# Performance work log

Measured on AMD Instinct MI355X. Metric: run time of the kernel, lower is better.

Reference implementation:

```python
import jax, jax.numpy as jnp
import numpy as np
import math

DIM = 1024
NUM_HEADS = 8
HEAD_DIM = DIM // NUM_HEADS
B, T, K_T, K_A, K_P = 8, 1024, 512, 64, 64
LN_EPS = 1e-5


def setup_inputs() -> dict:
    key = jax.random.key(0)
    ks = jax.random.split(key, 16)
    s = 1.0 / math.sqrt(DIM)
    inp = {
        "x": jax.random.normal(ks[0], (B, T, DIM), jnp.float32),
        "h_t": jax.random.normal(ks[1], (B, K_T, DIM), jnp.float32),
        "h_a": jax.random.normal(ks[2], (B, K_A, DIM), jnp.float32),
        "p": jax.random.normal(ks[3], (B, K_P, DIM), jnp.float32),
        "Wq": jax.random.normal(ks[4], (DIM, DIM), jnp.float32) * s,
        "bq": jnp.zeros((DIM,), jnp.float32),
        "Wk": jax.random.normal(ks[5], (DIM, DIM), jnp.float32) * s,
        "bk": jnp.zeros((DIM,), jnp.float32),
        "Wv": jax.random.normal(ks[6], (DIM, DIM), jnp.float32) * s,
        "bv": jnp.zeros((DIM,), jnp.float32),
        "Wo": jax.random.normal(ks[7], (DIM, DIM), jnp.float32) * s,
        "bo": jnp.zeros((DIM,), jnp.float32),
        "gating_factor": jnp.zeros((1,), jnp.float32) + 0.1,
        "ln_g": jnp.ones((DIM,), jnp.float32),
        "ln_b": jnp.zeros((DIM,), jnp.float32),
        "Wf": jax.random.normal(ks[8], (DIM, DIM), jnp.float32) * s,
        "bf": jnp.zeros((DIM,), jnp.float32),
    }
    return inp


def _heads(t):  # [B,S,C] -> [B,H,S,D]
    Bx, S, _ = t.shape
    return t.reshape(Bx, S, NUM_HEADS, HEAD_DIM).transpose(0, 2, 1, 3)


def reference(x, h_t, h_a, p, Wq, bq, Wk, bk, Wv, bv, Wo, bo,
              gating_factor, ln_g, ln_b, Wf, bf):
    ratio_g = jnp.tanh(gating_factor)  # shape (1,)
    h = jnp.concatenate([h_a, p], axis=1)  # [B, K_a, C]

    q = _heads(x @ Wq.T + bq)                 # [B,H,T,D]
    k_tok = _heads(x @ Wk.T + bk)
    v_tok = _heads(x @ Wv.T + bv)
    k_act = _heads(h @ Wk.T + bk)
    v_act = _heads(h @ Wv.T + bv)
    k_tsk = _heads(h_t @ Wk.T + bk)
    v_tsk = _heads(h_t @ Wv.T + bv)

    s_tok = jnp.einsum('bhtd,bhsd->bhts', q, k_tok)
    s_act = jnp.einsum('bhtd,bhsd->bhts', q, k_act)
    s_tsk = jnp.einsum('bhtd,bhsd->bhts', q, k_tsk) * ratio_g
    scores = jnp.concatenate([s_tok, s_act, s_tsk], axis=-1) / math.sqrt(HEAD_DIM)
    attn = jax.nn.softmax(scores, axis=-1)  # [B,H,T,T+Ka+Kt]

    v_all = jnp.concatenate([v_tok, v_act, v_tsk], axis=2)  # [B,H,S_all,D]
    out = jnp.einsum('bhts,bhsd->bhtd', attn, v_all)
    out = out.transpose(0, 2, 1, 3).reshape(x.shape)  # [B,T,C]
    out = out @ Wo.T + bo

    y = out + x
    mu = jnp.mean(y, axis=-1, keepdims=True)
    var = jnp.mean(jnp.square(y - mu), axis=-1, keepdims=True)
    y = (y - mu) * jax.lax.rsqrt(var + LN_EPS) * ln_g + ln_b
    y = y @ Wf.T + bf
    return jax.nn.relu(y)
```

## Files before the change

### kernel.cpp

```cpp
#include <hip/hip_runtime.h>
#include <hip/hip_bf16.h>
#include <math.h>

typedef unsigned short u16;
typedef __attribute__((ext_vector_type(8))) short s16x8;
typedef __attribute__((ext_vector_type(4))) float f32x4;
typedef __attribute__((ext_vector_type(16))) float f32x16;
typedef __attribute__((ext_vector_type(4))) unsigned short u16x4;

__device__ __forceinline__ u16 f2bf(float f) {
  union { float f; unsigned u; } v; v.f = f;
  unsigned r = (v.u + 0x7FFFu + ((v.u >> 16) & 1u)) >> 16;
  return (u16)r;
}

__device__ __forceinline__ void gload16(const void* g, void* l) {
  __builtin_amdgcn_global_load_lds((const __attribute__((address_space(1))) unsigned int*)g,
                                   (__attribute__((address_space(3))) unsigned int*)l, 16, 0, 0);
}

__device__ __forceinline__ unsigned cvt_pk_bf16(float a, float b) {
  unsigned r;
  asm("v_cvt_pk_bf16_f32 %0, %1, %2" : "=v"(r) : "v"(a), "v"(b));
  return r;
}


__global__ __launch_bounds__(256) void cvt_weights(
    const float* __restrict__ wq, const float* __restrict__ wk, const float* __restrict__ wv,
    const float* __restrict__ wo, const float* __restrict__ wf,
    u16* __restrict__ wqkv, u16* __restrict__ wobf, u16* __restrict__ wfbf)
{
  int i = blockIdx.x * 256 + threadIdx.x;
  int which = i >> 18;
  int idx = i & 262143;
  const float* src = which==0 ? wq : which==1 ? wk : which==2 ? wv : which==3 ? wo : wf;
  float4 v = ((const float4*)src)[idx];
  u16x4 o = { f2bf(v.x), f2bf(v.y), f2bf(v.z), f2bf(v.w) };
  u16* dst = which < 3 ? (wqkv + (size_t)which*1048576) : (which==3 ? wobf : wfbf);
  ((u16x4*)dst)[idx] = o;
}

__global__ __launch_bounds__(256) void build_m(
    const float* __restrict__ x, const float* __restrict__ ht,
    const float* __restrict__ ha, const float* __restrict__ p,
    u16* __restrict__ M)
{
  int row = blockIdx.x; int t = threadIdx.x;
  int b = row / 1664, s = row % 1664;
  const float* src;
  if (s < 1024)      src = x  + (size_t)(b*1024 + s)*1024;
  else if (s < 1088) src = ha + (size_t)(b*64 + (s-1024))*1024;
  else if (s < 1152) src = p  + (size_t)(b*64 + (s-1088))*1024;
  else               src = ht + (size_t)(b*512 + (s-1152))*1024;
  float4 v = ((const float4*)src)[t];
  u16x4 o = { f2bf(v.x), f2bf(v.y), f2bf(v.z), f2bf(v.w) };
  ((u16x4*)(M + (size_t)row*1024))[t] = o;
}


template<int EPI>
__global__ __launch_bounds__(256) void gemm_bt(
    const u16* __restrict__ A, const u16* __restrict__ Bw, int K,
    const float* __restrict__ bias0, const float* __restrict__ bias1, const float* __restrict__ bias2,
    const void* p0, void* p1, void* p2, void* p3)
{
  __shared__ __align__(16) u16 As[128*32];
  __shared__ __align__(16) u16 Bs[128*32];
  const int tid = threadIdx.x;
  const int l = tid & 63;
  const int w = tid >> 6;
  const int m0 = blockIdx.x * 128;
  const int n0 = blockIdx.y * 128;

  if constexpr (EPI == 0) {
    if (n0 < 1024 && (m0 % 1664) >= 1024) return;
  }

  const int wr = w >> 1, wc = w & 1;
  const int l15 = l & 15, lg = l >> 4;

  f32x4 acc[4][4];
  #pragma unroll
  for (int i=0;i<4;++i)
    #pragma unroll
    for (int j=0;j<4;++j) acc[i][j] = (f32x4){0,0,0,0};

  const int kiters = K >> 5;
  for (int kt = 0; kt < kiters; ++kt) {
    __syncthreads();
    #pragma unroll
    for (int c = 0; c < 2; ++c) {
      const int rbase = w*32 + c*16;
      const int rl = rbase + (l >> 2);
      const int kb = kt*32 + (l & 3)*8;
      gload16(A  + (size_t)(m0 + rl)*K + kb, (void*)(As + rbase*32));
      gload16(Bw + (size_t)(n0 + rl)*K + kb, (void*)(Bs + rbase*32));
    }
    __syncthreads();
    s16x8 av[4];
    #pragma unroll
    for (int mi=0;mi<4;++mi)
      av[mi] = *(const s16x8*)(As + (wr*64 + mi*16 + l15)*32 + lg*8);
    #pragma unroll
    for (int ni=0;ni<4;++ni) {
      s16x8 bv = *(const s16x8*)(Bs + (wc*64 + ni*16 + l15)*32 + lg*8);
      #pragma unroll
      for (int mi=0;mi<4;++mi)
        acc[mi][ni] = __builtin_amdgcn_mfma_f32_16x16x32_bf16(av[mi], bv, acc[mi][ni], 0,0,0);
    }
  }

  float ratio = 0.f;
  if constexpr (EPI == 0) ratio = tanhf(((const float*)p0)[0]);

  #pragma unroll
  for (int mi=0;mi<4;++mi) {
    #pragma unroll
    for (int ni=0;ni<4;++ni) {
      #pragma unroll
      for (int r=0;r<4;++r) {
        const int row = m0 + wr*64 + mi*16 + lg*4 + r;
        const int col = n0 + wc*64 + ni*16 + l15;
        if constexpr (EPI == 0) {
          const int b = row / 1664, s = row % 1664;
          if (col < 1024) {
            float v = acc[mi][ni][r] + bias0[col];
            if (s < 1024)
              ((u16*)p1)[(size_t)(b*1024 + s)*1024 + col] = f2bf(v * 0.08838834764831845f);
          } else if (col < 2048) {
            float v = acc[mi][ni][r] + bias1[col-1024];
            if (s >= 1152) v *= ratio;
            ((u16*)p2)[(size_t)row*1024 + (col-1024)] = f2bf(v);
          } else {
            float v = acc[mi][ni][r] + bias2[col-2048];
            ((u16*)p3)[(size_t)row*1024 + (col-2048)] = f2bf(v);
          }
        } else if constexpr (EPI == 1) {
          float v = acc[mi][ni][r] + bias0[col] + ((const float*)p0)[(size_t)row*1024 + col];
          ((float*)p1)[(size_t)row*1024 + col] = v;
        } else {
          float v = acc[mi][ni][r] + bias0[col];
          ((float*)p1)[(size_t)row*1024 + col] = fmaxf(v, 0.f);
        }
      }
    }
  }
}


__global__ __launch_bounds__(256) void vtrans(
    const u16* __restrict__ V, u16* __restrict__ Vt)
{
  __shared__ u16 Ls[64][68];
  const int st = blockIdx.x, dt = blockIdx.y, b = blockIdx.z;
  const int t = threadIdx.x;
  const int rq = t >> 4, c4 = t & 15;
  #pragma unroll
  for (int i=0;i<4;++i) {
    const int r = i*16 + rq;
    u16x4 v = *(const u16x4*)(V + ((size_t)(b*1664 + st*64 + r))*1024 + dt*64 + c4*4);
    Ls[r][c4*4+0] = v[0]; Ls[r][c4*4+1] = v[1]; Ls[r][c4*4+2] = v[2]; Ls[r][c4*4+3] = v[3];
  }
  __syncthreads();
  #pragma unroll
  for (int i=0;i<4;++i) {
    const int dr = i*16 + rq;
    u16x4 ov = { Ls[c4*4+0][dr], Ls[c4*4+1][dr], Ls[c4*4+2][dr], Ls[c4*4+3][dr] };
    *(u16x4*)(Vt + ((size_t)(b*1024 + dt*64 + dr))*1664 + st*64 + c4*4) = ov;
  }
}


__global__ __launch_bounds__(256, 2) void flash_attn(
    const u16* __restrict__ Q, const u16* __restrict__ Kb, const u16* __restrict__ Vtg,
    u16* __restrict__ O)
{
  __shared__ __align__(16) u16 Kl[2][64*128];
  __shared__ __align__(16) u16 Vl[2][128*64];

  const int tid = threadIdx.x;
  const int l = tid & 63;
  const int w = tid >> 6;
  const int l31 = l & 31;
  const int hi = l >> 5;
  const int bh = blockIdx.x & 63;
  const int qt = blockIdx.x >> 6;
  const int b = bh >> 3, h = bh & 7;
  const int colh = h * 128;
  const int q0 = qt*128 + w*32;

  s16x8 qf[8];
  {
    const size_t qrow = (size_t)(b*1024 + q0 + l31)*1024 + colh;
    #pragma unroll
    for (int kc=0;kc<8;++kc)
      qf[kc] = *(const s16x8*)(Q + qrow + kc*16 + hi*8);
  }

  f32x16 oacc[4];
  #pragma unroll
  for (int dt2=0;dt2<4;++dt2)
    #pragma unroll
    for (int i=0;i<16;++i) oacc[dt2][i] = 0.f;
  float m_run = -INFINITY, l_run = 0.f;

  const size_t kbase  = (size_t)(b*1664)*1024 + colh;
  const size_t vtbase = (size_t)(b*1024 + colh)*1664;

  auto stage = [&](int st, int nb) {
    const int s0 = st*64;
    #pragma unroll
    for (int i=0;i<4;++i) {
      const int e = i*256 + tid;
      const int sl = e >> 4, c = e & 15;
      const int g = (c & 8) | ((c ^ sl) & 7);
      gload16(Kb + kbase + (size_t)(s0 + sl)*1024 + g*8,
              (void*)(Kl[nb] + (i*256 + w*64)*8));
    }
    #pragma unroll
    for (int i=0;i<4;++i) {
      const int e = i*256 + tid;
      const int d = e >> 3, c3 = e & 7;
      const int g3 = (c3 ^ d) & 7;
      gload16(Vtg + vtbase + (size_t)d*1664 + s0 + g3*8,
              (void*)(Vl[nb] + (i*256 + w*64)*8));
    }
  };

  stage(0, 0);
  __syncthreads();
  int cur = 0;

  for (int st=0; st<26; ++st) {
    if (st + 1 < 26) stage(st + 1, cur ^ 1);

    f32x16 sacc[2];
    #pragma unroll
    for (int stile=0; stile<2; ++stile) {
      #pragma unroll
      for (int i=0;i<16;++i) sacc[stile][i] = 0.f;
      #pragma unroll
      for (int kc=0; kc<8; ++kc) {
        const int sl = stile*32 + l31;
        const int gc = kc*2 + hi;
        const int cl = (gc & 8) | ((gc ^ sl) & 7);
        s16x8 kf = *(const s16x8*)(Kl[cur] + sl*128 + cl*8);
        sacc[stile] = __builtin_amdgcn_mfma_f32_32x32x16_bf16(kf, qf[kc], sacc[stile], 0,0,0);
      }
    }

    float tm[8];
    #pragma unroll
    for (int i=0;i<8;++i)
      tm[i] = fmaxf(fmaxf(sacc[0][i], sacc[0][i+8]), fmaxf(sacc[1][i], sacc[1][i+8]));
    float pm = fmaxf(fmaxf(fmaxf(tm[0],tm[1]), fmaxf(tm[2],tm[3])),
                     fmaxf(fmaxf(tm[4],tm[5]), fmaxf(tm[6],tm[7])));
    pm = fmaxf(pm, __shfl_xor(pm, 32));

    if (__any(pm > m_run + 8.f)) {
      const float mnew = fmaxf(m_run, pm);
      const float alpha = __expf(m_run - mnew);
      m_run = mnew;
      l_run *= alpha;
      #pragma unroll
      for (int r=0;r<16;++r) {
        const int qr = (r&3) + 8*(r>>2) + 4*hi;
        const float ar = __shfl(alpha, qr);
        #pragma unroll
        for (int dt2=0;dt2<4;++dt2) oacc[dt2][r] *= ar;
      }
    }

    float ps = 0.f;
    #pragma unroll
    for (int stile=0; stile<2; ++stile)
      #pragma unroll
      for (int i=0;i<16;++i) {
        const float v = __expf(sacc[stile][i] - m_run);
        sacc[stile][i] = v;
        ps += v;
      }
    ps += __shfl_xor(ps, 32);
    l_run += ps;

    s16x8 pf[4];
    #pragma unroll
    for (int kc2=0; kc2<4; ++kc2) {
      const int stile = kc2 >> 1;
      const int rb = (kc2 & 1) * 8;
      const unsigned A = cvt_pk_bf16(sacc[stile][rb+0], sacc[stile][rb+1]);
      const unsigned B = cvt_pk_bf16(sacc[stile][rb+2], sacc[stile][rb+3]);
      const unsigned C = cvt_pk_bf16(sacc[stile][rb+4], sacc[stile][rb+5]);
      const unsigned D = cvt_pk_bf16(sacc[stile][rb+6], sacc[stile][rb+7]);
      const unsigned x1 = (unsigned)__shfl_xor((int)(hi ? A : C), 32);
      const unsigned x2 = (unsigned)__shfl_xor((int)(hi ? B : D), 32);
      union { unsigned u[4]; s16x8 v; } fr;
      fr.u[0] = hi ? x1 : A;
      fr.u[1] = hi ? x2 : B;
      fr.u[2] = hi ? C : x1;
      fr.u[3] = hi ? D : x2;
      pf[kc2] = fr.v;
    }

    #pragma unroll
    for (int dt2=0; dt2<4; ++dt2) {
      const int d = dt2*32 + l31;
      #pragma unroll
      for (int kc2=0; kc2<4; ++kc2) {
        const int g3 = kc2*2 + hi;
        const int cl3 = (g3 ^ d) & 7;
        s16x8 vf = *(const s16x8*)(Vl[cur] + d*64 + cl3*8);
        oacc[dt2] = __builtin_amdgcn_mfma_f32_32x32x16_bf16(pf[kc2], vf, oacc[dt2], 0,0,0);
      }
    }

    __syncthreads();
    cur ^= 1;
  }

  const float linv = 1.f / l_run;
  #pragma unroll
  for (int r=0;r<16;++r) {
    const int qr = (r&3) + 8*(r>>2) + 4*hi;
    const float lr = __shfl(linv, qr);
    const size_t row = (size_t)(b*1024 + q0 + qr)*1024 + colh;
    #pragma unroll
    for (int dt2=0;dt2<4;++dt2)
      O[row + dt2*32 + l31] = f2bf(oacc[dt2][r] * lr);
  }
}


__global__ __launch_bounds__(256) void ln_kernel(
    const float* __restrict__ y, const float* __restrict__ g, const float* __restrict__ bb,
    u16* __restrict__ out)
{
  const int row = blockIdx.x, t = threadIdx.x;
  float4 v = ((const float4*)y)[row*256 + t];
  float s  = v.x + v.y + v.z + v.w;
  float s2 = v.x*v.x + v.y*v.y + v.z*v.z + v.w*v.w;
  #pragma unroll
  for (int off=1; off<64; off<<=1) { s += __shfl_xor(s, off); s2 += __shfl_xor(s2, off); }
  __shared__ float ps[4], ps2[4];
  const int w = t >> 6;
  if ((t & 63) == 0) { ps[w] = s; ps2[w] = s2; }
  __syncthreads();
  s  = ps[0] + ps[1] + ps[2] + ps[3];
  s2 = ps2[0] + ps2[1] + ps2[2] + ps2[3];
  const float mu = s * (1.f/1024.f);
  const float var = s2 * (1.f/1024.f) - mu*mu;
  const float rs = rsqrtf(var + 1e-5f);
  float4 gg = ((const float4*)g)[t];
  float4 bv = ((const float4*)bb)[t];
  u16x4 o = { f2bf((v.x-mu)*rs*gg.x + bv.x),
              f2bf((v.y-mu)*rs*gg.y + bv.y),
              f2bf((v.z-mu)*rs*gg.z + bv.z),
              f2bf((v.w-mu)*rs*gg.w + bv.w) };
  ((u16x4*)out)[row*256 + t] = o;
}


extern "C" void kernel_launch(void* const* d_in, const int* in_sizes, int n_in,
                              void* d_out, int out_size, void* d_ws, size_t ws_size,
                              hipStream_t stream)
{
  (void)in_sizes; (void)n_in; (void)out_size; (void)ws_size;
  const float* x   = (const float*)d_in[0];
  const float* ht  = (const float*)d_in[1];
  const float* ha  = (const float*)d_in[2];
  const float* pp  = (const float*)d_in[3];
  const float* Wq  = (const float*)d_in[4];
  const float* bq  = (const float*)d_in[5];
  const float* Wk  = (const float*)d_in[6];
  const float* bk  = (const float*)d_in[7];
  const float* Wv  = (const float*)d_in[8];
  const float* bv  = (const float*)d_in[9];
  const float* Wo  = (const float*)d_in[10];
  const float* bo  = (const float*)d_in[11];
  const float* gat = (const float*)d_in[12];
  const float* lng = (const float*)d_in[13];
  const float* lnb = (const float*)d_in[14];
  const float* Wf  = (const float*)d_in[15];
  const float* bfp = (const float*)d_in[16];
  float* out = (float*)d_out;

  char* ws = (char*)d_ws;
  size_t off = 0;
  auto alloc = [&](size_t bytes) { void* r = ws + off; off += (bytes + 255) & ~255ull; return r; };
  u16* M    = (u16*)alloc(13312ull*1024*2);
  u16* Wqkv = (u16*)alloc(3072ull*1024*2);
  u16* Wobf = (u16*)alloc(1024ull*1024*2);
  u16* Wfbf = (u16*)alloc(1024ull*1024*2);
  u16* Qb   = (u16*)alloc(8192ull*1024*2);
  u16* Kb2  = (u16*)alloc(13312ull*1024*2);
  u16* Vb2  = (u16*)alloc(13312ull*1024*2);
  u16* Ab   = (u16*)alloc(8192ull*1024*2);
  u16* Vtg  = M;
  float* Y  = (float*)M;
  u16* Ln   = Qb;

  hipLaunchKernelGGL(cvt_weights, dim3(5120), dim3(256), 0, stream,
                     Wq, Wk, Wv, Wo, Wf, Wqkv, Wobf, Wfbf);
  hipLaunchKernelGGL(build_m, dim3(13312), dim3(256), 0, stream, x, ht, ha, pp, M);
  hipLaunchKernelGGL((gemm_bt<0>), dim3(104, 24), dim3(256), 0, stream,
                     M, Wqkv, 1024, bq, bk, bv,
                     (const void*)gat, (void*)Qb, (void*)Kb2, (void*)Vb2);
  hipLaunchKernelGGL(vtrans, dim3(26, 16, 8), dim3(256), 0, stream, Vb2, Vtg);
  hipLaunchKernelGGL(flash_attn, dim3(512), dim3(256), 0, stream, Qb, Kb2, Vtg, Ab);
  hipLaunchKernelGGL((gemm_bt<1>), dim3(64, 8), dim3(256), 0, stream,
                     Ab, Wobf, 1024, bo, nullptr, nullptr,
                     (const void*)x, (void*)Y, nullptr, nullptr);
  hipLaunchKernelGGL(ln_kernel, dim3(8192), dim3(256), 0, stream, Y, lng, lnb, Ln);
  hipLaunchKernelGGL((gemm_bt<2>), dim3(64, 8), dim3(256), 0, stream,
                     Ln, Wfbf, 1024, bfp, nullptr, nullptr,
                     nullptr, (void*)out, nullptr, nullptr);
}
```

Measured before the change: 489.6 us.

## Replace QKV projection with 256x256 double-buffered pipelined MFMA GEMM kernel

Adds a dedicated QKV projection kernel that uses 256x256 tiles with 512 threads, a two-stage LDS ring buffer with XOR-swizzled layout, and interleaved prefetch/compute phases with explicit waitcnt/barrier and setprio. It also remaps blocks with a swizzle and skips Q tiles that fall entirely in the non-token rows. The aim is to raise MFMA utilisation and data reuse over the previous 128x128 single-buffered GEMM and to hide global load latency. The cost is heavy hand-tuned synchronisation that is fragile and sensitive to register pressure and occupancy, with some wasted work on tiles that only partly overlap the token rows.

```diff
diff --git a/kernel.cpp b/kernel.cpp
--- a/kernel.cpp
+++ b/kernel.cpp
@@ -59,11 +59,142 @@
 }
 
 
+#define PHASE(D, QM, QN, STAGE_STMT, ENDSYNC)                                    \
+  {                                                                              \
+    s16x8 af_[4][2], bf_[2][2];                                                  \
+    _Pragma("unroll")                                                            \
+    for (int mi2=0; mi2<4; ++mi2) {                                              \
+      const int r = wm*128 + (QM*4+mi2)*16 + l15;                                \
+      _Pragma("unroll")                                                          \
+      for (int ks=0; ks<2; ++ks)                                                 \
+        af_[mi2][ks] = *(const s16x8*)(As[D] + r*64 + (((ks*4+lg) ^ (r&7))<<3)); \
+    }                                                                            \
+    _Pragma("unroll")                                                            \
+    for (int ni2=0; ni2<2; ++ni2) {                                              \
+      const int r = wn*64 + (QN*2+ni2)*16 + l15;                                 \
+      _Pragma("unroll")                                                          \
+      for (int ks=0; ks<2; ++ks)                                                 \
+        bf_[ni2][ks] = *(const s16x8*)(Bs[D] + r*64 + (((ks*4+lg) ^ (r&7))<<3)); \
+    }                                                                            \
+    STAGE_STMT;                                                                  \
+    __builtin_amdgcn_s_barrier();                                                \
+    asm volatile("s_waitcnt lgkmcnt(0)" ::: "memory");                           \
+    __builtin_amdgcn_s_setprio(1);                                               \
+    _Pragma("unroll")                                                            \
+    for (int mi2=0; mi2<4; ++mi2)                                                \
+      _Pragma("unroll")                                                          \
+      for (int ni2=0; ni2<2; ++ni2)                                              \
+        _Pragma("unroll")                                                        \
+        for (int ks=0; ks<2; ++ks)                                               \
+          acc[QM*4+mi2][QN*2+ni2] = __builtin_amdgcn_mfma_f32_16x16x32_bf16(     \
+              af_[mi2][ks], bf_[ni2][ks], acc[QM*4+mi2][QN*2+ni2], 0,0,0);       \
+    __builtin_amdgcn_s_setprio(0);                                               \
+    ENDSYNC;                                                                     \
+  }
+
+__global__ __launch_bounds__(512, 2) void gemm256_qkv(
+    const u16* __restrict__ A, const u16* __restrict__ Bw,
+    const float* __restrict__ bias_q, const float* __restrict__ bias_k,
+    const float* __restrict__ bias_v, const float* __restrict__ gat,
+    u16* __restrict__ Qb, u16* __restrict__ Kb, u16* __restrict__ Vb)
+{
+  __shared__ __align__(16) u16 As[2][256*64];
+  __shared__ __align__(16) u16 Bs[2][256*64];
+
+  const int tid = threadIdx.x;
+  const int l = tid & 63;
+  const int w = tid >> 6;
+  const int wm = w >> 2, wn = w & 3;
+  const int l15 = l & 15, lg = l >> 4;
+  const int w8 = w * 8;
+
+  const int b0 = blockIdx.x;
+  const int swz = (b0 & 7) * 78 + (b0 >> 3);
+  const int mt = swz % 52, nt = swz / 52;
+  const int m0 = mt * 256, n0 = nt * 256;
+
+  if (n0 < 1024) {
+    const int s0 = m0 % 1664;
+    if (s0 >= 1024 && s0 <= 1408) return;
+  }
+
+  auto stA = [&](int d, int h, int kt) {
+    #pragma unroll
+    for (int i=0;i<2;++i) {
+      const int r0 = i*128 + h*64 + w8;
+      const int r  = r0 + (l >> 3);
+      const int sck = (l & 7) ^ (r & 7);
+      gload16(A + (size_t)(m0 + r)*1024 + kt*64 + sck*8, (void*)(As[d] + r0*64));
+    }
+  };
+  auto stB = [&](int d, int h, int kt) {
+    #pragma unroll
+    for (int i=0;i<2;++i) {
+      const int blk = i*2 + (w>>2);
+      const int r0 = (w&3)*8 + blk*64 + h*32;
+      const int r  = r0 + (l >> 3);
+      const int sck = (l & 7) ^ (r & 7);
+      gload16(Bw + (size_t)(n0 + r)*1024 + kt*64 + sck*8, (void*)(Bs[d] + r0*64));
+    }
+  };
+
+  f32x4 acc[8][4];
+  #pragma unroll
+  for (int i=0;i<8;++i)
+    #pragma unroll
+    for (int j=0;j<4;++j) acc[i][j] = (f32x4){0,0,0,0};
+
+  stB(0,0,0); stA(0,1,0); stA(0,0,0); stB(0,1,0); stB(1,0,1); stA(1,1,1);
+  asm volatile("s_waitcnt vmcnt(4)\ns_barrier" ::: "memory");
+
+  for (int t = 0; t < 16; ++t) {
+    const int d = t & 1;
+    const int e = d ^ 1;
+    PHASE(d, 0, 0, if (t+1 < 16) stA(e, 0, t+1), __builtin_amdgcn_s_barrier())
+    PHASE(d, 1, 0, if (t+1 < 16) stB(e, 1, t+1),
+          asm volatile("s_waitcnt vmcnt(8)\ns_barrier" ::: "memory"))
+    PHASE(d, 1, 1, if (t+2 < 16) stB(d, 0, t+2), __builtin_amdgcn_s_barrier())
+    PHASE(d, 0, 1, if (t+2 < 16) stA(d, 1, t+2), )
+    if (t <= 13)      asm volatile("s_waitcnt vmcnt(6)\ns_barrier" ::: "memory");
+    else if (t == 14) asm volatile("s_waitcnt vmcnt(0)\ns_barrier" ::: "memory");
+    else              __builtin_amdgcn_s_barrier();
+  }
+
+  const float ratio = tanhf(gat[0]);
+  #pragma unroll
+  for (int mi=0;mi<8;++mi) {
+    #pragma unroll
+    for (int ni=0;ni<4;++ni) {
+      #pragma unroll
+      for (int rr=0;rr<4;++rr) {
+        const int row = m0 + wm*128 + mi*16 + lg*4 + rr;
+        const int col = n0 + wn*64 + ni*16 + l15;
+        const int b = row / 1664, s = row % 1664;
+        const float a = acc[mi][ni][rr];
+        if (col < 1024) {
+          if (s < 1024) {
+            float v = a + bias_q[col];
+            Qb[(size_t)(b*1024 + s)*1024 + col] = f2bf(v * 0.08838834764831845f);
+          }
+        } else if (col < 2048) {
+          float v = a + bias_k[col-1024];
+          if (s >= 1152) v *= ratio;
+          Kb[(size_t)row*1024 + (col-1024)] = f2bf(v);
+        } else {
+          float v = a + bias_v[col-2048];
+          Vb[(size_t)row*1024 + (col-2048)] = f2bf(v);
+        }
+      }
+    }
+  }
+}
+
+
 template<int EPI>
 __global__ __launch_bounds__(256) void gemm_bt(
     const u16* __restrict__ A, const u16* __restrict__ Bw, int K,
-    const float* __restrict__ bias0, const float* __restrict__ bias1, const float* __restrict__ bias2,
-    const void* p0, void* p1, void* p2, void* p3)
+    const float* __restrict__ bias0,
+    const void* p0, void* p1)
 {
   __shared__ __align__(16) u16 As[128*32];
   __shared__ __align__(16) u16 Bs[128*32];
@@ -73,10 +204,6 @@
   const int m0 = blockIdx.x * 128;
   const int n0 = blockIdx.y * 128;
 
-  if constexpr (EPI == 0) {
-    if (n0 < 1024 && (m0 % 1664) >= 1024) return;
-  }
-
   const int wr = w >> 1, wc = w & 1;
   const int l15 = l & 15, lg = l >> 4;
 
@@ -111,9 +238,6 @@
     }
   }
 
-  float ratio = 0.f;
-  if constexpr (EPI == 0) ratio = tanhf(((const float*)p0)[0]);
-
   #pragma unroll
   for (int mi=0;mi<4;++mi) {
     #pragma unroll
@@ -122,21 +246,7 @@
       for (int r=0;r<4;++r) {
         const int row = m0 + wr*64 + mi*16 + lg*4 + r;
         const int col = n0 + wc*64 + ni*16 + l15;
-        if constexpr (EPI == 0) {
-          const int b = row / 1664, s = row % 1664;
-          if (col < 1024) {
-            float v = acc[mi][ni][r] + bias0[col];
-            if (s < 1024)
-              ((u16*)p1)[(size_t)(b*1024 + s)*1024 + col] = f2bf(v * 0.08838834764831845f);
-          } else if (col < 2048) {
-            float v = acc[mi][ni][r] + bias1[col-1024];
-            if (s >= 1152) v *= ratio;
-            ((u16*)p2)[(size_t)row*1024 + (col-1024)] = f2bf(v);
-          } else {
-            float v = acc[mi][ni][r] + bias2[col-2048];
-            ((u16*)p3)[(size_t)row*1024 + (col-2048)] = f2bf(v);
-          }
-        } else if constexpr (EPI == 1) {
+        if constexpr (EPI == 1) {
           float v = acc[mi][ni][r] + bias0[col] + ((const float*)p0)[(size_t)row*1024 + col];
           ((float*)p1)[(size_t)row*1024 + col] = v;
         } else {
@@ -403,16 +513,13 @@
   hipLaunchKernelGGL(cvt_weights, dim3(5120), dim3(256), 0, stream,
                      Wq, Wk, Wv, Wo, Wf, Wqkv, Wobf, Wfbf);
   hipLaunchKernelGGL(build_m, dim3(13312), dim3(256), 0, stream, x, ht, ha, pp, M);
-  hipLaunchKernelGGL((gemm_bt<0>), dim3(104, 24), dim3(256), 0, stream,
-                     M, Wqkv, 1024, bq, bk, bv,
-                     (const void*)gat, (void*)Qb, (void*)Kb2, (void*)Vb2);
+  hipLaunchKernelGGL(gemm256_qkv, dim3(624), dim3(512), 0, stream,
+                     M, Wqkv, bq, bk, bv, gat, Qb, Kb2, Vb2);
   hipLaunchKernelGGL(vtrans, dim3(26, 16, 8), dim3(256), 0, stream, Vb2, Vtg);
   hipLaunchKernelGGL(flash_attn, dim3(512), dim3(256), 0, stream, Qb, Kb2, Vtg, Ab);
   hipLaunchKernelGGL((gemm_bt<1>), dim3(64, 8), dim3(256), 0, stream,
-                     Ab, Wobf, 1024, bo, nullptr, nullptr,
-                     (const void*)x, (void*)Y, nullptr, nullptr);
+                     Ab, Wobf, 1024, bo, (const void*)x, (void*)Y);
   hipLaunchKernelGGL(ln_kernel, dim3(8192), dim3(256), 0, stream, Y, lng, lnb, Ln);
   hipLaunchKernelGGL((gemm_bt<2>), dim3(64, 8), dim3(256), 0, stream,
-                     Ln, Wfbf, 1024, bfp, nullptr, nullptr,
-                     nullptr, (void*)out, nullptr, nullptr);
-}
+                     Ln, Wfbf, 1024, bfp, nullptr, (void*)out);
+}
```

Measured after the change: 487.0 us. About the same (-0.5%).

## Add triple-buffered swizzled QKV GEMM with XCD-aware tile mapping

Applied to the files above, without the earlier changes.

Replaces the generic QKV projection GEMM with a dedicated kernel. It uses triple-buffered LDS staging with asynchronous global-to-LDS loads issued two k-steps ahead, an XOR-swizzled LDS layout to avoid bank conflicts, s_setprio around the MFMA block, and a block-to-tile remap that groups M tiles per XCD for L2 reuse. The goal is to hide load latency and remove the two full barriers per k-iteration in the old loop. In exchange it uses more LDS per block, which can limit occupancy.

```diff
diff --git a/kernel.cpp b/kernel.cpp
--- a/kernel.cpp
+++ b/kernel.cpp
@@ -59,11 +59,124 @@
 }
 
 
+__global__ __launch_bounds__(256, 3) void gemm128_qkv(
+    const u16* __restrict__ A, const u16* __restrict__ Bw,
+    const float* __restrict__ bias_q, const float* __restrict__ bias_k,
+    const float* __restrict__ bias_v, const float* __restrict__ gat,
+    u16* __restrict__ Qb, u16* __restrict__ Kb, u16* __restrict__ Vb)
+{
+  __shared__ __align__(16) u16 As3[3][128*32];
+  __shared__ __align__(16) u16 Bs3[3][128*32];
+
+  const int tid = threadIdx.x;
+  const int l = tid & 63;
+  const int w = tid >> 6;
+  const int wr = w >> 1, wc = w & 1;
+  const int l15 = l & 15, lg = l >> 4;
+
+  const int b0 = blockIdx.x;
+  const int xcd = b0 & 7;
+  const int loc = b0 >> 3;
+  const int g = loc / 52, r5 = loc % 52;
+  const int mt = xcd*13 + (r5 % 13);
+  const int nt = g*4 + (r5 / 13);
+  const int m0 = mt * 128, n0 = nt * 128;
+
+  if (n0 < 1024 && (m0 % 1664) >= 1024) return;
+
+  auto stage = [&](int kt, int sb) {
+    #pragma unroll
+    for (int i=0;i<2;++i) {
+      const int e = i*256 + tid;
+      const int rr = e >> 2, c2 = e & 3;
+      const int gch = c2 ^ ((rr >> 1) & 3);
+      gload16(A + (size_t)(m0 + rr)*1024 + kt*32 + gch*8,
+              (void*)(As3[sb] + (i*256 + w*64)*8));
+    }
+    #pragma unroll
+    for (int i=0;i<2;++i) {
+      const int e = i*256 + tid;
+      const int rr = e >> 2, c2 = e & 3;
+      const int gch = c2 ^ ((rr >> 1) & 3);
+      gload16(Bw + (size_t)(n0 + rr)*1024 + kt*32 + gch*8,
+              (void*)(Bs3[sb] + (i*256 + w*64)*8));
+    }
+  };
+
+  f32x4 acc[4][4];
+  #pragma unroll
+  for (int i=0;i<4;++i)
+    #pragma unroll
+    for (int j=0;j<4;++j) acc[i][j] = (f32x4){0,0,0,0};
+
+  stage(0, 0); stage(1, 1);
+  asm volatile("s_waitcnt vmcnt(4)\ns_barrier" ::: "memory");
+
+  int cur = 0;
+  for (int t = 0; t < 32; ++t) {
+    const int sb = cur >= 1 ? cur - 1 : 2;
+    if (t + 2 < 32) stage(t + 2, sb);
+
+    s16x8 af[4], bf[4];
+    #pragma unroll
+    for (int mi=0;mi<4;++mi) {
+      const int rr = wr*64 + mi*16 + l15;
+      af[mi] = *(const s16x8*)(As3[cur] + rr*32 + ((lg ^ ((rr>>1)&3))<<3));
+    }
+    #pragma unroll
+    for (int ni=0;ni<4;++ni) {
+      const int rr = wc*64 + ni*16 + l15;
+      bf[ni] = *(const s16x8*)(Bs3[cur] + rr*32 + ((lg ^ ((rr>>1)&3))<<3));
+    }
+
+    __builtin_amdgcn_s_setprio(1);
+    #pragma unroll
+    for (int mi=0;mi<4;++mi)
+      #pragma unroll
+      for (int ni=0;ni<4;++ni)
+        acc[mi][ni] = __builtin_amdgcn_mfma_f32_16x16x32_bf16(af[mi], bf[ni], acc[mi][ni], 0,0,0);
+    __builtin_amdgcn_s_setprio(0);
+
+    if (t < 30)       asm volatile("s_waitcnt vmcnt(4)\ns_barrier" ::: "memory");
+    else if (t == 30) asm volatile("s_waitcnt vmcnt(0)\ns_barrier" ::: "memory");
+    cur = cur == 2 ? 0 : cur + 1;
+  }
+
+  const float ratio = tanhf(gat[0]);
+  #pragma unroll
+  for (int mi=0;mi<4;++mi) {
+    #pragma unroll
+    for (int ni=0;ni<4;++ni) {
+      #pragma unroll
+      for (int rr=0;rr<4;++rr) {
+        const int row = m0 + wr*64 + mi*16 + lg*4 + rr;
+        const int col = n0 + wc*64 + ni*16 + l15;
+        const int b = row / 1664, s = row % 1664;
+        const float a = acc[mi][ni][rr];
+        if (col < 1024) {
+          if (s < 1024) {
+            float v = a + bias_q[col];
+            Qb[(size_t)(b*1024 + s)*1024 + col] = f2bf(v * 0.08838834764831845f);
+          }
+        } else if (col < 2048) {
+          float v = a + bias_k[col-1024];
+          if (s >= 1152) v *= ratio;
+          Kb[(size_t)row*1024 + (col-1024)] = f2bf(v);
+        } else {
+          float v = a + bias_v[col-2048];
+          Vb[(size_t)row*1024 + (col-2048)] = f2bf(v);
+        }
+      }
+    }
+  }
+}
+
+
 template<int EPI>
 __global__ __launch_bounds__(256) void gemm_bt(
     const u16* __restrict__ A, const u16* __restrict__ Bw, int K,
-    const float* __restrict__ bias0, const float* __restrict__ bias1, const float* __restrict__ bias2,
-    const void* p0, void* p1, void* p2, void* p3)
+    const float* __restrict__ bias0,
+    const void* p0, void* p1)
 {
   __shared__ __align__(16) u16 As[128*32];
   __shared__ __align__(16) u16 Bs[128*32];
@@ -73,10 +186,6 @@
   const int m0 = blockIdx.x * 128;
   const int n0 = blockIdx.y * 128;
 
-  if constexpr (EPI == 0) {
-    if (n0 < 1024 && (m0 % 1664) >= 1024) return;
-  }
-
   const int wr = w >> 1, wc = w & 1;
   const int l15 = l & 15, lg = l >> 4;
 
@@ -111,9 +220,6 @@
     }
   }
 
-  float ratio = 0.f;
-  if constexpr (EPI == 0) ratio = tanhf(((const float*)p0)[0]);
-
   #pragma unroll
   for (int mi=0;mi<4;++mi) {
     #pragma unroll
@@ -122,21 +228,7 @@
       for (int r=0;r<4;++r) {
         const int row = m0 + wr*64 + mi*16 + lg*4 + r;
         const int col = n0 + wc*64 + ni*16 + l15;
-        if constexpr (EPI == 0) {
-          const int b = row / 1664, s = row % 1664;
-          if (col < 1024) {
-            float v = acc[mi][ni][r] + bias0[col];
-            if (s < 1024)
-              ((u16*)p1)[(size_t)(b*1024 + s)*1024 + col] = f2bf(v * 0.08838834764831845f);
-          } else if (col < 2048) {
-            float v = acc[mi][ni][r] + bias1[col-1024];
-            if (s >= 1152) v *= ratio;
-            ((u16*)p2)[(size_t)row*1024 + (col-1024)] = f2bf(v);
-          } else {
-            float v = acc[mi][ni][r] + bias2[col-2048];
-            ((u16*)p3)[(size_t)row*1024 + (col-2048)] = f2bf(v);
-          }
-        } else if constexpr (EPI == 1) {
+        if constexpr (EPI == 1) {
           float v = acc[mi][ni][r] + bias0[col] + ((const float*)p0)[(size_t)row*1024 + col];
           ((float*)p1)[(size_t)row*1024 + col] = v;
         } else {
@@ -403,16 +495,13 @@
   hipLaunchKernelGGL(cvt_weights, dim3(5120), dim3(256), 0, stream,
                      Wq, Wk, Wv, Wo, Wf, Wqkv, Wobf, Wfbf);
   hipLaunchKernelGGL(build_m, dim3(13312), dim3(256), 0, stream, x, ht, ha, pp, M);
-  hipLaunchKernelGGL((gemm_bt<0>), dim3(104, 24), dim3(256), 0, stream,
-                     M, Wqkv, 1024, bq, bk, bv,
-                     (const void*)gat, (void*)Qb, (void*)Kb2, (void*)Vb2);
+  hipLaunchKernelGGL(gemm128_qkv, dim3(2496), dim3(256), 0, stream,
+                     M, Wqkv, bq, bk, bv, gat, Qb, Kb2, Vb2);
   hipLaunchKernelGGL(vtrans, dim3(26, 16, 8), dim3(256), 0, stream, Vb2, Vtg);
   hipLaunchKernelGGL(flash_attn, dim3(512), dim3(256), 0, stream, Qb, Kb2, Vtg, Ab);
   hipLaunchKernelGGL((gemm_bt<1>), dim3(64, 8), dim3(256), 0, stream,
-                     Ab, Wobf, 1024, bo, nullptr, nullptr,
-                     (const void*)x, (void*)Y, nullptr, nullptr);
+                     Ab, Wobf, 1024, bo, (const void*)x, (void*)Y);
   hipLaunchKernelGGL(ln_kernel, dim3(8192), dim3(256), 0, stream, Y, lng, lnb, Ln);
   hipLaunchKernelGGL((gemm_bt<2>), dim3(64, 8), dim3(256), 0, stream,
-                     Ln, Wfbf, 1024, bfp, nullptr, nullptr,
-                     nullptr, (void*)out, nullptr, nullptr);
-}
+                     Ln, Wfbf, 1024, bfp, nullptr, (void*)out);
+}
```

New measurement: 425.9 us. 13.0% less time.

## Double-buffer GEMM LDS tiles with swizzle and XCD-aware block mapping

Applied to the files above, without the earlier changes.

Rewrites the bf16 GEMM kernel so the next K-slice is loaded into a second LDS buffer while MFMAs run on the current one, which halves the barriers per iteration. It also XOR-swizzles the LDS layout to reduce bank conflicts, raises MFMA wave priority, and remaps the flat block index so each XCD works on a contiguous group of M tiles, improving L2 reuse. LDS use doubles, which may lower occupancy, and K is now hard-coded to 1024.

```diff
diff --git a/kernel.cpp b/kernel.cpp
--- a/kernel.cpp
+++ b/kernel.cpp
@@ -60,25 +60,53 @@
 
 
 template<int EPI>
-__global__ __launch_bounds__(256) void gemm_bt(
-    const u16* __restrict__ A, const u16* __restrict__ Bw, int K,
-    const float* __restrict__ bias0, const float* __restrict__ bias1, const float* __restrict__ bias2,
-    const void* p0, void* p1, void* p2, void* p3)
-{
-  __shared__ __align__(16) u16 As[128*32];
-  __shared__ __align__(16) u16 Bs[128*32];
+__global__ __launch_bounds__(256, 5) void gemm128(
+    const u16* __restrict__ A, const u16* __restrict__ Bw,
+    const float* __restrict__ bias0, const float* __restrict__ bias1,
+    const float* __restrict__ bias2, const float* __restrict__ gat,
+    void* o0, void* o1, void* o2, const float* __restrict__ resid,
+    int mpx, int ng)
+{
+  __shared__ __align__(16) u16 As2[2][128*32];
+  __shared__ __align__(16) u16 Bs2[2][128*32];
+
   const int tid = threadIdx.x;
   const int l = tid & 63;
   const int w = tid >> 6;
-  const int m0 = blockIdx.x * 128;
-  const int n0 = blockIdx.y * 128;
+  const int wr = w >> 1, wc = w & 1;
+  const int l15 = l & 15, lg = l >> 4;
+
+  const int b0 = blockIdx.x;
+  const int xcd = b0 & 7;
+  const int loc = b0 >> 3;
+  const int chunk = mpx * ng;
+  const int g = loc / chunk, r5 = loc % chunk;
+  const int mt = xcd*mpx + (r5 % mpx);
+  const int nt = g*ng + (r5 / mpx);
+  const int m0 = mt * 128, n0 = nt * 128;
 
   if constexpr (EPI == 0) {
     if (n0 < 1024 && (m0 % 1664) >= 1024) return;
   }
 
-  const int wr = w >> 1, wc = w & 1;
-  const int l15 = l & 15, lg = l >> 4;
+  auto stage = [&](int kt, int sb) {
+    #pragma unroll
+    for (int i=0;i<2;++i) {
+      const int e = i*256 + tid;
+      const int rr = e >> 2, c2 = e & 3;
+      const int gch = c2 ^ ((rr >> 1) & 3);
+      gload16(A + (size_t)(m0 + rr)*1024 + kt*32 + gch*8,
+              (void*)(As2[sb] + (i*256 + w*64)*8));
+    }
+    #pragma unroll
+    for (int i=0;i<2;++i) {
+      const int e = i*256 + tid;
+      const int rr = e >> 2, c2 = e & 3;
+      const int gch = c2 ^ ((rr >> 1) & 3);
+      gload16(Bw + (size_t)(n0 + rr)*1024 + kt*32 + gch*8,
+              (void*)(Bs2[sb] + (i*256 + w*64)*8));
+    }
+  };
 
   f32x4 acc[4][4];
   #pragma unroll
@@ -86,62 +114,69 @@
     #pragma unroll
     for (int j=0;j<4;++j) acc[i][j] = (f32x4){0,0,0,0};
 
-  const int kiters = K >> 5;
-  for (int kt = 0; kt < kiters; ++kt) {
-    __syncthreads();
-    #pragma unroll
-    for (int c = 0; c < 2; ++c) {
-      const int rbase = w*32 + c*16;
-      const int rl = rbase + (l >> 2);
-      const int kb = kt*32 + (l & 3)*8;
-      gload16(A  + (size_t)(m0 + rl)*K + kb, (void*)(As + rbase*32));
-      gload16(Bw + (size_t)(n0 + rl)*K + kb, (void*)(Bs + rbase*32));
-    }
-    __syncthreads();
-    s16x8 av[4];
+  stage(0, 0);
+  asm volatile("s_waitcnt vmcnt(0)\ns_barrier" ::: "memory");
+
+  for (int t = 0; t < 32; ++t) {
+    const int cur = t & 1;
+    if (t + 1 < 32) stage(t + 1, cur ^ 1);
+
+    s16x8 af[4], bf[4];
+    #pragma unroll
+    for (int mi=0;mi<4;++mi) {
+      const int rr = wr*64 + mi*16 + l15;
+      af[mi] = *(const s16x8*)(As2[cur] + rr*32 + ((lg ^ ((rr>>1)&3))<<3));
+    }
+    #pragma unroll
+    for (int ni=0;ni<4;++ni) {
+      const int rr = wc*64 + ni*16 + l15;
+      bf[ni] = *(const s16x8*)(Bs2[cur] + rr*32 + ((lg ^ ((rr>>1)&3))<<3));
+    }
+
+    __builtin_amdgcn_s_setprio(1);
     #pragma unroll
     for (int mi=0;mi<4;++mi)
-      av[mi] = *(const s16x8*)(As + (wr*64 + mi*16 + l15)*32 + lg*8);
+      #pragma unroll
+      for (int ni=0;ni<4;++ni)
+        acc[mi][ni] = __builtin_amdgcn_mfma_f32_16x16x32_bf16(af[mi], bf[ni], acc[mi][ni], 0,0,0);
+    __builtin_amdgcn_s_setprio(0);
+
+    if (t < 31) asm volatile("s_waitcnt vmcnt(0)\ns_barrier" ::: "memory");
+  }
+
+  float ratio = 0.f;
+  if constexpr (EPI == 0) ratio = tanhf(gat[0]);
+
+  #pragma unroll
+  for (int mi=0;mi<4;++mi) {
     #pragma unroll
     for (int ni=0;ni<4;++ni) {
-      s16x8 bv = *(const s16x8*)(Bs + (wc*64 + ni*16 + l15)*32 + lg*8);
-      #pragma unroll
-      for (int mi=0;mi<4;++mi)
-        acc[mi][ni] = __builtin_amdgcn_mfma_f32_16x16x32_bf16(av[mi], bv, acc[mi][ni], 0,0,0);
-    }
-  }
-
-  float ratio = 0.f;
-  if constexpr (EPI == 0) ratio = tanhf(((const float*)p0)[0]);
-
-  #pragma unroll
-  for (int mi=0;mi<4;++mi) {
-    #pragma unroll
-    for (int ni=0;ni<4;++ni) {
-      #pragma unroll
-      for (int r=0;r<4;++r) {
-        const int row = m0 + wr*64 + mi*16 + lg*4 + r;
+      #pragma unroll
+      for (int rr=0;rr<4;++rr) {
+        const int row = m0 + wr*64 + mi*16 + lg*4 + rr;
         const int col = n0 + wc*64 + ni*16 + l15;
+        const float a = acc[mi][ni][rr];
         if constexpr (EPI == 0) {
           const int b = row / 1664, s = row % 1664;
           if (col < 1024) {
-            float v = acc[mi][ni][r] + bias0[col];
-            if (s < 1024)
-              ((u16*)p1)[(size_t)(b*1024 + s)*1024 + col] = f2bf(v * 0.08838834764831845f);
+            if (s < 1024) {
+              float v = a + bias0[col];
+              ((u16*)o0)[(size_t)(b*1024 + s)*1024 + col] = f2bf(v * 0.08838834764831845f);
+            }
           } else if (col < 2048) {
-            float v = acc[mi][ni][r] + bias1[col-1024];
+            float v = a + bias1[col-1024];
             if (s >= 1152) v *= ratio;
-            ((u16*)p2)[(size_t)row*1024 + (col-1024)] = f2bf(v);
+            ((u16*)o1)[(size_t)row*1024 + (col-1024)] = f2bf(v);
           } else {
-            float v = acc[mi][ni][r] + bias2[col-2048];
-            ((u16*)p3)[(size_t)row*1024 + (col-2048)] = f2bf(v);
+            float v = a + bias2[col-2048];
+            ((u16*)o2)[(size_t)row*1024 + (col-2048)] = f2bf(v);
           }
         } else if constexpr (EPI == 1) {
-          float v = acc[mi][ni][r] + bias0[col] + ((const float*)p0)[(size_t)row*1024 + col];
-          ((float*)p1)[(size_t)row*1024 + col] = v;
+          float v = a + bias0[col] + resid[(size_t)row*1024 + col];
+          ((float*)o0)[(size_t)row*1024 + col] = v;
         } else {
-          float v = acc[mi][ni][r] + bias0[col];
-          ((float*)p1)[(size_t)row*1024 + col] = fmaxf(v, 0.f);
+          float v = a + bias0[col];
+          ((float*)o0)[(size_t)row*1024 + col] = fmaxf(v, 0.f);
         }
       }
     }
@@ -403,16 +438,16 @@
   hipLaunchKernelGGL(cvt_weights, dim3(5120), dim3(256), 0, stream,
                      Wq, Wk, Wv, Wo, Wf, Wqkv, Wobf, Wfbf);
   hipLaunchKernelGGL(build_m, dim3(13312), dim3(256), 0, stream, x, ht, ha, pp, M);
-  hipLaunchKernelGGL((gemm_bt<0>), dim3(104, 24), dim3(256), 0, stream,
-                     M, Wqkv, 1024, bq, bk, bv,
-                     (const void*)gat, (void*)Qb, (void*)Kb2, (void*)Vb2);
+  hipLaunchKernelGGL((gemm128<0>), dim3(2496), dim3(256), 0, stream,
+                     M, Wqkv, bq, bk, bv, gat,
+                     (void*)Qb, (void*)Kb2, (void*)Vb2, nullptr, 13, 4);
   hipLaunchKernelGGL(vtrans, dim3(26, 16, 8), dim3(256), 0, stream, Vb2, Vtg);
   hipLaunchKernelGGL(flash_attn, dim3(512), dim3(256), 0, stream, Qb, Kb2, Vtg, Ab);
-  hipLaunchKernelGGL((gemm_bt<1>), dim3(64, 8), dim3(256), 0, stream,
-                     Ab, Wobf, 1024, bo, nullptr, nullptr,
-                     (const void*)x, (void*)Y, nullptr, nullptr);
+  hipLaunchKernelGGL((gemm128<1>), dim3(512), dim3(256), 0, stream,
+                     Ab, Wobf, bo, nullptr, nullptr, nullptr,
+                     (void*)Y, nullptr, nullptr, x, 8, 8);
   hipLaunchKernelGGL(ln_kernel, dim3(8192), dim3(256), 0, stream, Y, lng, lnb, Ln);
-  hipLaunchKernelGGL((gemm_bt<2>), dim3(64, 8), dim3(256), 0, stream,
-                     Ln, Wfbf, 1024, bfp, nullptr, nullptr,
-                     nullptr, (void*)out, nullptr, nullptr);
-}
+  hipLaunchKernelGGL((gemm128<2>), dim3(512), dim3(256), 0, stream,
+                     Ln, Wfbf, bfp, nullptr, nullptr, nullptr,
+                     (void*)out, nullptr, nullptr, nullptr, 8, 8);
+}
```

Result: slower. 583.3 us (+19.1%).
